# Performance work log

Measured on AMD Instinct MI355X. Metric: run time of the kernel, lower is better.

The kernel has to match this reference:

```python
import jax, jax.numpy as jnp
import numpy as np

N_NODES = 50000
N_EDGES = 800000


def setup_inputs() -> dict:
    key = jax.random.key(0)
    k1, k2, k3, k4 = jax.random.split(key, 4)
    x = jax.random.normal(k1, (N_NODES, 128), dtype=jnp.float32)
    edge_index = jax.random.randint(k2, (2, N_EDGES), 0, N_NODES, dtype=jnp.int64)
    W1 = jax.random.normal(k3, (128, 64), dtype=jnp.float32) / np.sqrt(128.0)
    b1 = jnp.zeros((64,), dtype=jnp.float32)
    W2 = jax.random.normal(k4, (64, 40), dtype=jnp.float32) / np.sqrt(64.0)
    b2 = jnp.zeros((40,), dtype=jnp.float32)
    return {"x": x, "edge_index": edge_index, "W1": W1, "b1": b1, "W2": W2, "b2": b2}


def _gcn_norm(edge_index, n_nodes):
    # Add self-loops, then compute symmetric normalization D^{-1/2} A D^{-1/2}
    loop = jnp.arange(n_nodes, dtype=edge_index.dtype)
    row = jnp.concatenate([edge_index[0], loop])  # source
    col = jnp.concatenate([edge_index[1], loop])  # target
    ones = jnp.ones(row.shape[0], dtype=jnp.float32)
    deg = jax.ops.segment_sum(ones, col, num_segments=n_nodes)
    dinv = jnp.where(deg > 0, jax.lax.rsqrt(deg), 0.0)
    norm = dinv[row] * dinv[col]  # [E + N]
    return row, col, norm


def _gcn_conv(h, W, b, row, col, norm, n_nodes):
    hw = h @ W                         # transform first (smaller messages)
    msg = hw[row] * norm[:, None]      # gather + scale per edge
    agg = jax.ops.segment_sum(msg, col, num_segments=n_nodes)
    return agg + b


def reference(x, edge_index, W1, b1, W2, b2):
    n = x.shape[0]
    row, col, norm = _gcn_norm(edge_index, n)
    h = _gcn_conv(x, W1, b1, row, col, norm, n)
    h = jax.nn.relu(h)
    h = _gcn_conv(h, W2, b2, row, col, norm, n)
    return jax.nn.softmax(h, axis=-1)
```

## Files before the change

kernel.cpp:

```cpp
#include <hip/hip_runtime.h>

#define N_NODES 50000
#define N_EDGES 800000
#define F_IN   128
#define F_MID  64
#define F_OUT  40

#define SLICE_SHIFT 10
#define SLICE_SZ    1024
#define NSLICE      49
#define PCHUNKS     256
#define PCHUNK_E    ((N_EDGES + PCHUNKS - 1) / PCHUNKS)
#define NCOUNT      (NSLICE * PCHUNKS)


__global__ __launch_bounds__(256) void bucket_count(const int* __restrict__ ei,
                                                    int* __restrict__ counts) {
    __shared__ int cnt[NSLICE];
    if (threadIdx.x < NSLICE) cnt[threadIdx.x] = 0;
    __syncthreads();
    int e0 = blockIdx.x * PCHUNK_E;
    int e1 = e0 + PCHUNK_E; if (e1 > N_EDGES) e1 = N_EDGES;
    for (int e = e0 + threadIdx.x; e < e1; e += 256) {
        int c = ei[N_EDGES + e];
        atomicAdd(&cnt[c >> SLICE_SHIFT], 1);
    }
    __syncthreads();
    if (threadIdx.x < NSLICE) counts[threadIdx.x * PCHUNKS + blockIdx.x] = cnt[threadIdx.x];
}


__global__ __launch_bounds__(256) void sc_bsum(const int* __restrict__ counts, int* __restrict__ bsum) {
    int idx = blockIdx.x * 256 + threadIdx.x;
    int v = (idx < NCOUNT) ? counts[idx] : 0;
#pragma unroll
    for (int off = 32; off > 0; off >>= 1) v += __shfl_xor(v, off, 64);
    __shared__ int ws[4];
    if ((threadIdx.x & 63) == 0) ws[threadIdx.x >> 6] = v;
    __syncthreads();
    if (threadIdx.x == 0) bsum[blockIdx.x] = ws[0] + ws[1] + ws[2] + ws[3];
}

__global__ __launch_bounds__(64) void sc_bscan(const int* __restrict__ bsum, int* __restrict__ boff) {
    int tid = threadIdx.x;
    int v = (tid < NSLICE) ? bsum[tid] : 0;
    int inc = v;
#pragma unroll
    for (int s = 1; s < 64; s <<= 1) {
        int t = __shfl_up(inc, s, 64);
        if (tid >= s) inc += t;
    }
    if (tid < NSLICE) boff[tid] = inc - v;
}

__global__ __launch_bounds__(256) void sc_bscan2(const int* __restrict__ counts,
                                                 const int* __restrict__ boff,
                                                 int* __restrict__ choff) {
    int idx = blockIdx.x * 256 + threadIdx.x;
    int lane = threadIdx.x & 63, wv = threadIdx.x >> 6;
    int v = (idx < NCOUNT) ? counts[idx] : 0;
    int inc = v;
#pragma unroll
    for (int s = 1; s < 64; s <<= 1) {
        int t = __shfl_up(inc, s, 64);
        if (lane >= s) inc += t;
    }
    __shared__ int ws[4];
    if (lane == 63) ws[wv] = inc;
    __syncthreads();
    int off = boff[blockIdx.x];
    for (int w = 0; w < wv; ++w) off += ws[w];
    if (idx < NCOUNT) choff[idx] = off + inc - v;
}


__global__ __launch_bounds__(256) void bucket_scatter(const int* __restrict__ ei,
                                                      const int* __restrict__ choff,
                                                      int2* __restrict__ pairs) {
    __shared__ int cur[NSLICE];
    if (threadIdx.x < NSLICE) cur[threadIdx.x] = choff[threadIdx.x * PCHUNKS + blockIdx.x];
    __syncthreads();
    int e0 = blockIdx.x * PCHUNK_E;
    int e1 = e0 + PCHUNK_E; if (e1 > N_EDGES) e1 = N_EDGES;
    for (int e = e0 + threadIdx.x; e < e1; e += 256) {
        int r = ei[e];
        int c = ei[N_EDGES + e];
        int pos = atomicAdd(&cur[c >> SLICE_SHIFT], 1);
        pairs[pos] = make_int2(r, c);
    }
}


__global__ __launch_bounds__(1024) void slice_csr(const int2* __restrict__ pairs,
                                                  const int* __restrict__ choff,
                                                  int* __restrict__ rowptr,
                                                  float* __restrict__ dinv,
                                                  int* __restrict__ srcs) {
    __shared__ int hist[SLICE_SZ];
    __shared__ int wpart[16];
    int s = blockIdx.x;
    int base = choff[s * PCHUNKS];
    int end  = (s == NSLICE - 1) ? N_EDGES : choff[(s + 1) * PCHUNKS];
    int tid = threadIdx.x;
    hist[tid] = 0;
    __syncthreads();
    for (int i = base + tid; i < end; i += 1024)
        atomicAdd(&hist[pairs[i].y & (SLICE_SZ - 1)], 1);
    __syncthreads();
    int v = hist[tid];
    int lane = tid & 63, wv = tid >> 6;
    int inc = v;
#pragma unroll
    for (int st = 1; st < 64; st <<= 1) {
        int t = __shfl_up(inc, st, 64);
        if (lane >= st) inc += t;
    }
    if (lane == 63) wpart[wv] = inc;
    __syncthreads();
    int woff = 0;
    for (int w = 0; w < wv; ++w) woff += wpart[w];
    int ex = woff + inc - v;
    hist[tid] = ex;
    int node = s * SLICE_SZ + tid;
    if (node < N_NODES) {
        rowptr[node] = base + ex;
        dinv[node]   = rsqrtf((float)v + 1.0f);
    }
    if (node == N_NODES - 1) rowptr[N_NODES] = N_EDGES;
    __syncthreads();
    for (int i = base + tid; i < end; i += 1024) {
        int2 p = pairs[i];
        int pos = atomicAdd(&hist[p.y & (SLICE_SZ - 1)], 1);
        srcs[base + pos] = p.x;
    }
}


__global__ __launch_bounds__(256) void gemm1_kernel(const float* __restrict__ x,
                                                    const float* __restrict__ W1,
                                                    const float* __restrict__ dinv,
                                                    float* __restrict__ hw1s) {
    __shared__ float sW[F_IN * F_MID];
    __shared__ float sX[64][68];
    int tid = threadIdx.x;
    const float4* W4 = (const float4*)W1;
    float4* sW4 = (float4*)sW;
    for (int i = tid; i < F_IN * F_MID / 4; i += 256) sW4[i] = W4[i];

    int row0 = blockIdx.x * 64;
    int tx = tid & 15, ty = tid >> 4;
    int c0 = tx * 4, r0 = ty * 4;
    float acc[4][4] = {};

    for (int p = 0; p < 2; ++p) {
        __syncthreads();
#pragma unroll
        for (int it = 0; it < 4; ++it) {
            int i = (tid + it * 256) * 4;
            int r = i >> 6, k = i & 63;
            float4 v = make_float4(0.f, 0.f, 0.f, 0.f);
            if (row0 + r < N_NODES)
                v = *(const float4*)&x[(size_t)(row0 + r) * F_IN + p * 64 + k];
            *(float4*)&sX[r][k] = v;
        }
        __syncthreads();
        const float* sWp = sW + p * 64 * F_MID;
#pragma unroll 4
        for (int k = 0; k < 64; ++k) {
            float4 w = *(const float4*)&sWp[k * F_MID + c0];
            float a0 = sX[r0 + 0][k];
            float a1 = sX[r0 + 1][k];
            float a2 = sX[r0 + 2][k];
            float a3 = sX[r0 + 3][k];
            acc[0][0] = fmaf(a0, w.x, acc[0][0]); acc[0][1] = fmaf(a0, w.y, acc[0][1]);
            acc[0][2] = fmaf(a0, w.z, acc[0][2]); acc[0][3] = fmaf(a0, w.w, acc[0][3]);
            acc[1][0] = fmaf(a1, w.x, acc[1][0]); acc[1][1] = fmaf(a1, w.y, acc[1][1]);
            acc[1][2] = fmaf(a1, w.z, acc[1][2]); acc[1][3] = fmaf(a1, w.w, acc[1][3]);
            acc[2][0] = fmaf(a2, w.x, acc[2][0]); acc[2][1] = fmaf(a2, w.y, acc[2][1]);
            acc[2][2] = fmaf(a2, w.z, acc[2][2]); acc[2][3] = fmaf(a2, w.w, acc[2][3]);
            acc[3][0] = fmaf(a3, w.x, acc[3][0]); acc[3][1] = fmaf(a3, w.y, acc[3][1]);
            acc[3][2] = fmaf(a3, w.z, acc[3][2]); acc[3][3] = fmaf(a3, w.w, acc[3][3]);
        }
    }
#pragma unroll
    for (int j = 0; j < 4; ++j) {
        int row = row0 + r0 + j;
        if (row < N_NODES) {
            float d = dinv[row];
            float4 o = make_float4(acc[j][0] * d, acc[j][1] * d, acc[j][2] * d, acc[j][3] * d);
            *(float4*)&hw1s[(size_t)row * F_MID + c0] = o;
        }
    }
}


__global__ __launch_bounds__(256) void gather1_kernel(const int* __restrict__ rowptr,
                                                      const int* __restrict__ srcs,
                                                      const float* __restrict__ hw1s,
                                                      const float* __restrict__ dinv,
                                                      const float* __restrict__ b1,
                                                      float* __restrict__ h) {
    int n = blockIdx.x * 4 + (threadIdx.x >> 6);
    int lane = threadIdx.x & 63;
    if (n >= N_NODES) return;
    int s = rowptr[n], e = rowptr[n + 1];
    float acc = 0.f;
    for (int base = s; base < e; base += 64) {
        int cnt = e - base; if (cnt > 64) cnt = 64;
        int ms = (lane < cnt) ? srcs[base + lane] : 0;
        int j = 0;
        for (; j + 4 <= cnt; j += 4) {
            int i0 = __shfl(ms, j, 64),     i1 = __shfl(ms, j + 1, 64);
            int i2 = __shfl(ms, j + 2, 64), i3 = __shfl(ms, j + 3, 64);
            float v0 = hw1s[(size_t)i0 * F_MID + lane];
            float v1 = hw1s[(size_t)i1 * F_MID + lane];
            float v2 = hw1s[(size_t)i2 * F_MID + lane];
            float v3 = hw1s[(size_t)i3 * F_MID + lane];
            acc += v0 + v1 + v2 + v3;
        }
        for (; j < cnt; ++j) {
            int i0 = __shfl(ms, j, 64);
            acc += hw1s[(size_t)i0 * F_MID + lane];
        }
    }
    float d = dinv[n];
    float v = fmaf(d, acc + hw1s[(size_t)n * F_MID + lane], b1[lane]);
    h[(size_t)n * F_MID + lane] = fmaxf(v, 0.f);
}


__global__ __launch_bounds__(256) void gemm2_kernel(const float* __restrict__ h,
                                                    const float* __restrict__ W2,
                                                    const float* __restrict__ dinv,
                                                    float* __restrict__ hw2s) {
    __shared__ float sW[F_MID * F_OUT];
    for (int i = threadIdx.x; i < F_MID * F_OUT; i += 256) sW[i] = W2[i];
    __syncthreads();
    int idx = blockIdx.x * 256 + threadIdx.x;
    if (idx >= N_NODES * F_OUT) return;
    int r = idx / F_OUT;
    int c = idx % F_OUT;
    float acc = 0.f;
#pragma unroll
    for (int k = 0; k < F_MID; ++k) acc = fmaf(h[(size_t)r * F_MID + k], sW[k * F_OUT + c], acc);
    hw2s[idx] = acc * dinv[r];
}


__global__ __launch_bounds__(256) void gather2_softmax_kernel(const int* __restrict__ rowptr,
                                                              const int* __restrict__ srcs,
                                                              const float* __restrict__ hw2s,
                                                              const float* __restrict__ dinv,
                                                              const float* __restrict__ b2,
                                                              float* __restrict__ out) {
    int n = blockIdx.x * 4 + (threadIdx.x >> 6);
    int lane = threadIdx.x & 63;
    if (n >= N_NODES) return;
    int s = rowptr[n], e = rowptr[n + 1];
    float acc = 0.f;
    for (int base = s; base < e; base += 64) {
        int cnt = e - base; if (cnt > 64) cnt = 64;
        int ms = (lane < cnt) ? srcs[base + lane] : 0;
        int j = 0;
        for (; j + 4 <= cnt; j += 4) {
            int i0 = __shfl(ms, j, 64),     i1 = __shfl(ms, j + 1, 64);
            int i2 = __shfl(ms, j + 2, 64), i3 = __shfl(ms, j + 3, 64);
            if (lane < F_OUT) {
                float v0 = hw2s[(size_t)i0 * F_OUT + lane];
                float v1 = hw2s[(size_t)i1 * F_OUT + lane];
                float v2 = hw2s[(size_t)i2 * F_OUT + lane];
                float v3 = hw2s[(size_t)i3 * F_OUT + lane];
                acc += v0 + v1 + v2 + v3;
            }
        }
        for (; j < cnt; ++j) {
            int i0 = __shfl(ms, j, 64);
            if (lane < F_OUT) acc += hw2s[(size_t)i0 * F_OUT + lane];
        }
    }
    float d = dinv[n];
    float v = -3.402823466e38f;
    if (lane < F_OUT)
        v = fmaf(d, acc + hw2s[(size_t)n * F_OUT + lane], b2[lane]);
    float m = v;
#pragma unroll
    for (int off = 32; off > 0; off >>= 1) m = fmaxf(m, __shfl_xor(m, off, 64));
    float p = (lane < F_OUT) ? __expf(v - m) : 0.f;
    float su = p;
#pragma unroll
    for (int off = 32; off > 0; off >>= 1) su += __shfl_xor(su, off, 64);
    if (lane < F_OUT) out[(size_t)n * F_OUT + lane] = p / su;
}


extern "C" void kernel_launch(void* const* d_in, const int* in_sizes, int n_in,
                              void* d_out, int out_size, void* d_ws, size_t ws_size,
                              hipStream_t stream) {
    const float* x  = (const float*)d_in[0];
    const int*   ei = (const int*)d_in[1];
    const float* W1 = (const float*)d_in[2];
    const float* b1 = (const float*)d_in[3];
    const float* W2 = (const float*)d_in[4];
    const float* b2 = (const float*)d_in[5];
    float* out = (float*)d_out;

    char* ws = (char*)d_ws;
    size_t off = 0;
    auto alloc = [&](size_t bytes) -> void* {
        void* p = ws + off;
        off += (bytes + 255) & ~(size_t)255;
        return p;
    };
    int*   counts = (int*)  alloc(NCOUNT * sizeof(int));
    int*   bsum   = (int*)  alloc(NSLICE * sizeof(int));
    int*   boff   = (int*)  alloc(NSLICE * sizeof(int));
    int*   choff  = (int*)  alloc(NCOUNT * sizeof(int));
    int2*  pairs  = (int2*) alloc((size_t)N_EDGES * sizeof(int2));
    int*   rowptr = (int*)  alloc((N_NODES + 1) * sizeof(int));
    float* dinv   = (float*)alloc(N_NODES * sizeof(float));
    int*   srcs   = (int*)  alloc((size_t)N_EDGES * sizeof(int));
    float* hw1s   = (float*)alloc((size_t)N_NODES * F_MID * sizeof(float));
    float* h      = (float*)alloc((size_t)N_NODES * F_MID * sizeof(float));
    float* hw2s   = (float*)alloc((size_t)N_NODES * F_OUT * sizeof(float));

    bucket_count  <<<PCHUNKS, 256, 0, stream>>>(ei, counts);
    sc_bsum       <<<NSLICE, 256, 0, stream>>>(counts, bsum);
    sc_bscan      <<<1, 64, 0, stream>>>(bsum, boff);
    sc_bscan2     <<<NSLICE, 256, 0, stream>>>(counts, boff, choff);
    bucket_scatter<<<PCHUNKS, 256, 0, stream>>>(ei, choff, pairs);
    slice_csr     <<<NSLICE, 1024, 0, stream>>>(pairs, choff, rowptr, dinv, srcs);
    gemm1_kernel  <<<(N_NODES + 63) / 64, 256, 0, stream>>>(x, W1, dinv, hw1s);
    gather1_kernel<<<(N_NODES + 3) / 4, 256, 0, stream>>>(rowptr, srcs, hw1s, dinv, b1, h);
    gemm2_kernel  <<<(N_NODES * F_OUT + 255) / 256, 256, 0, stream>>>(h, W2, dinv, hw2s);
    gather2_softmax_kernel<<<(N_NODES + 3) / 4, 256, 0, stream>>>(rowptr, srcs, hw2s, dinv, b2, out);
}
```

Baseline: 224.5 us.

## Use smaller CSR slices, pack edge pairs into one int, unroll gathers by eight

The bucket slice size drops from 1024 to 256 nodes, so the per-slice CSR build launches 196 blocks of 256 threads instead of 49 blocks of 1024. This spreads the build across more compute units. The scan kernels are resized to match, and the block-offset scan now handles up to 256 slices with a cross-wave step. Edge pairs are packed into a single int (source in the low 16 bits, local target in the upper bits), which halves scatter and read traffic but relies on node ids fitting in 16 bits. Both gather kernels unroll the neighbor loop to eight loads per step to keep more memory requests in flight.

```diff
diff --git a/kernel.cpp b/kernel.cpp
--- a/kernel.cpp
+++ b/kernel.cpp
@@ -6,12 +6,13 @@
 #define F_MID  64
 #define F_OUT  40
 
-#define SLICE_SHIFT 10
-#define SLICE_SZ    1024
-#define NSLICE      49
+#define SLICE_SHIFT 8
+#define SLICE_SZ    256
+#define NSLICE      196
 #define PCHUNKS     256
 #define PCHUNK_E    ((N_EDGES + PCHUNKS - 1) / PCHUNKS)
 #define NCOUNT      (NSLICE * PCHUNKS)
+
 
 
 __global__ __launch_bounds__(256) void bucket_count(const int* __restrict__ ei,
@@ -41,16 +42,22 @@
     if (threadIdx.x == 0) bsum[blockIdx.x] = ws[0] + ws[1] + ws[2] + ws[3];
 }
 
-__global__ __launch_bounds__(64) void sc_bscan(const int* __restrict__ bsum, int* __restrict__ boff) {
+__global__ __launch_bounds__(256) void sc_bscan(const int* __restrict__ bsum, int* __restrict__ boff) {
     int tid = threadIdx.x;
+    int lane = tid & 63, wv = tid >> 6;
     int v = (tid < NSLICE) ? bsum[tid] : 0;
     int inc = v;
 #pragma unroll
     for (int s = 1; s < 64; s <<= 1) {
         int t = __shfl_up(inc, s, 64);
-        if (tid >= s) inc += t;
-    }
-    if (tid < NSLICE) boff[tid] = inc - v;
+        if (lane >= s) inc += t;
+    }
+    __shared__ int ws[4];
+    if (lane == 63) ws[wv] = inc;
+    __syncthreads();
+    int woff = 0;
+    for (int w = 0; w < wv; ++w) woff += ws[w];
+    if (tid < NSLICE) boff[tid] = woff + inc - v;
 }
 
 __global__ __launch_bounds__(256) void sc_bscan2(const int* __restrict__ counts,
@@ -76,7 +83,7 @@
 
 __global__ __launch_bounds__(256) void bucket_scatter(const int* __restrict__ ei,
                                                       const int* __restrict__ choff,
-                                                      int2* __restrict__ pairs) {
+                                                      int* __restrict__ pairs) {
     __shared__ int cur[NSLICE];
     if (threadIdx.x < NSLICE) cur[threadIdx.x] = choff[threadIdx.x * PCHUNKS + blockIdx.x];
     __syncthreads();
@@ -86,26 +93,26 @@
         int r = ei[e];
         int c = ei[N_EDGES + e];
         int pos = atomicAdd(&cur[c >> SLICE_SHIFT], 1);
-        pairs[pos] = make_int2(r, c);
-    }
-}
-
-
-__global__ __launch_bounds__(1024) void slice_csr(const int2* __restrict__ pairs,
-                                                  const int* __restrict__ choff,
-                                                  int* __restrict__ rowptr,
-                                                  float* __restrict__ dinv,
-                                                  int* __restrict__ srcs) {
+        pairs[pos] = r | ((c & (SLICE_SZ - 1)) << 16);
+    }
+}
+
+
+__global__ __launch_bounds__(256) void slice_csr(const int* __restrict__ pairs,
+                                                 const int* __restrict__ choff,
+                                                 int* __restrict__ rowptr,
+                                                 float* __restrict__ dinv,
+                                                 int* __restrict__ srcs) {
     __shared__ int hist[SLICE_SZ];
-    __shared__ int wpart[16];
+    __shared__ int wpart[4];
     int s = blockIdx.x;
     int base = choff[s * PCHUNKS];
     int end  = (s == NSLICE - 1) ? N_EDGES : choff[(s + 1) * PCHUNKS];
     int tid = threadIdx.x;
     hist[tid] = 0;
     __syncthreads();
-    for (int i = base + tid; i < end; i += 1024)
-        atomicAdd(&hist[pairs[i].y & (SLICE_SZ - 1)], 1);
+    for (int i = base + tid; i < end; i += 256)
+        atomicAdd(&hist[pairs[i] >> 16], 1);
     __syncthreads();
     int v = hist[tid];
     int lane = tid & 63, wv = tid >> 6;
@@ -120,6 +127,7 @@
     int woff = 0;
     for (int w = 0; w < wv; ++w) woff += wpart[w];
     int ex = woff + inc - v;
+    __syncthreads();
     hist[tid] = ex;
     int node = s * SLICE_SZ + tid;
     if (node < N_NODES) {
@@ -128,10 +136,10 @@
     }
     if (node == N_NODES - 1) rowptr[N_NODES] = N_EDGES;
     __syncthreads();
-    for (int i = base + tid; i < end; i += 1024) {
-        int2 p = pairs[i];
-        int pos = atomicAdd(&hist[p.y & (SLICE_SZ - 1)], 1);
-        srcs[base + pos] = p.x;
+    for (int i = base + tid; i < end; i += 256) {
+        int p = pairs[i];
+        int pos = atomicAdd(&hist[p >> 16], 1);
+        srcs[base + pos] = p & 0xFFFF;
     }
 }
 
@@ -209,14 +217,20 @@
         int cnt = e - base; if (cnt > 64) cnt = 64;
         int ms = (lane < cnt) ? srcs[base + lane] : 0;
         int j = 0;
-        for (; j + 4 <= cnt; j += 4) {
+        for (; j + 8 <= cnt; j += 8) {
             int i0 = __shfl(ms, j, 64),     i1 = __shfl(ms, j + 1, 64);
             int i2 = __shfl(ms, j + 2, 64), i3 = __shfl(ms, j + 3, 64);
+            int i4 = __shfl(ms, j + 4, 64), i5 = __shfl(ms, j + 5, 64);
+            int i6 = __shfl(ms, j + 6, 64), i7 = __shfl(ms, j + 7, 64);
             float v0 = hw1s[(size_t)i0 * F_MID + lane];
             float v1 = hw1s[(size_t)i1 * F_MID + lane];
             float v2 = hw1s[(size_t)i2 * F_MID + lane];
             float v3 = hw1s[(size_t)i3 * F_MID + lane];
-            acc += v0 + v1 + v2 + v3;
+            float v4 = hw1s[(size_t)i4 * F_MID + lane];
+            float v5 = hw1s[(size_t)i5 * F_MID + lane];
+            float v6 = hw1s[(size_t)i6 * F_MID + lane];
+            float v7 = hw1s[(size_t)i7 * F_MID + lane];
+            acc += ((v0 + v1) + (v2 + v3)) + ((v4 + v5) + (v6 + v7));
         }
         for (; j < cnt; ++j) {
             int i0 = __shfl(ms, j, 64);
@@ -262,15 +276,21 @@
         int cnt = e - base; if (cnt > 64) cnt = 64;
         int ms = (lane < cnt) ? srcs[base + lane] : 0;
         int j = 0;
-        for (; j + 4 <= cnt; j += 4) {
+        for (; j + 8 <= cnt; j += 8) {
             int i0 = __shfl(ms, j, 64),     i1 = __shfl(ms, j + 1, 64);
             int i2 = __shfl(ms, j + 2, 64), i3 = __shfl(ms, j + 3, 64);
+            int i4 = __shfl(ms, j + 4, 64), i5 = __shfl(ms, j + 5, 64);
+            int i6 = __shfl(ms, j + 6, 64), i7 = __shfl(ms, j + 7, 64);
             if (lane < F_OUT) {
                 float v0 = hw2s[(size_t)i0 * F_OUT + lane];
                 float v1 = hw2s[(size_t)i1 * F_OUT + lane];
                 float v2 = hw2s[(size_t)i2 * F_OUT + lane];
                 float v3 = hw2s[(size_t)i3 * F_OUT + lane];
-                acc += v0 + v1 + v2 + v3;
+                float v4 = hw2s[(size_t)i4 * F_OUT + lane];
+                float v5 = hw2s[(size_t)i5 * F_OUT + lane];
+                float v6 = hw2s[(size_t)i6 * F_OUT + lane];
+                float v7 = hw2s[(size_t)i7 * F_OUT + lane];
+                acc += ((v0 + v1) + (v2 + v3)) + ((v4 + v5) + (v6 + v7));
             }
         }
         for (; j < cnt; ++j) {
@@ -315,7 +335,7 @@
     int*   bsum   = (int*)  alloc(NSLICE * sizeof(int));
     int*   boff   = (int*)  alloc(NSLICE * sizeof(int));
     int*   choff  = (int*)  alloc(NCOUNT * sizeof(int));
-    int2*  pairs  = (int2*) alloc((size_t)N_EDGES * sizeof(int2));
+    int*   pairs  = (int*)  alloc((size_t)N_EDGES * sizeof(int));
     int*   rowptr = (int*)  alloc((N_NODES + 1) * sizeof(int));
     float* dinv   = (float*)alloc(N_NODES * sizeof(float));
     int*   srcs   = (int*)  alloc((size_t)N_EDGES * sizeof(int));
@@ -324,11 +344,11 @@
     float* hw2s   = (float*)alloc((size_t)N_NODES * F_OUT * sizeof(float));
 
     bucket_count  <<<PCHUNKS, 256, 0, stream>>>(ei, counts);
-    sc_bsum       <<<NSLICE, 256, 0, stream>>>(counts, bsum);
-    sc_bscan      <<<1, 64, 0, stream>>>(bsum, boff);
-    sc_bscan2     <<<NSLICE, 256, 0, stream>>>(counts, boff, choff);
+    sc_bsum       <<<(NCOUNT + 255) / 256, 256, 0, stream>>>(counts, bsum);
+    sc_bscan      <<<1, 256, 0, stream>>>(bsum, boff);
+    sc_bscan2     <<<(NCOUNT + 255) / 256, 256, 0, stream>>>(counts, boff, choff);
     bucket_scatter<<<PCHUNKS, 256, 0, stream>>>(ei, choff, pairs);
-    slice_csr     <<<NSLICE, 1024, 0, stream>>>(pairs, choff, rowptr, dinv, srcs);
+    slice_csr     <<<NSLICE, 256, 0, stream>>>(pairs, choff, rowptr, dinv, srcs);
     gemm1_kernel  <<<(N_NODES + 63) / 64, 256, 0, stream>>>(x, W1, dinv, hw1s);
     gather1_kernel<<<(N_NODES + 3) / 4, 256, 0, stream>>>(rowptr, srcs, hw1s, dinv, b1, h);
     gemm2_kernel  <<<(N_NODES * F_OUT + 255) / 256, 256, 0, stream>>>(h, W2, dinv, hw2s);
```

New measurement: 217.2 us. 3.2% less time.
